# Kernel optimization log

Measured on AMD Instinct MI355X. Metric: run time of the kernel, lower is better.

## Reference

```python
import jax, jax.numpy as jnp
import numpy as np

B, S, D, H = 2, 2048, 1024, 16
DK = D // H


def setup_inputs() -> dict:
    key = jax.random.key(0)
    ks = jax.random.split(key, 12)
    sd = 1.0 / np.sqrt(D)
    inp = {
        "query": jax.random.normal(ks[0], (B, S, D), jnp.float32),
        "key": jax.random.normal(ks[1], (B, S, D), jnp.float32),
        "value": jax.random.normal(ks[2], (B, S, D), jnp.float32),
        # causal mask, broadcast over batch and heads: [1, 1, S, S]
        "mask": jnp.tril(jnp.ones((S, S), jnp.bool_))[None, None],
        "wq_w": jax.random.uniform(ks[3], (D, D), jnp.float32, -sd, sd),
        "wq_b": jax.random.uniform(ks[4], (D,), jnp.float32, -sd, sd),
        "wk_w": jax.random.uniform(ks[5], (D, D), jnp.float32, -sd, sd),
        "wk_b": jax.random.uniform(ks[6], (D,), jnp.float32, -sd, sd),
        "wv_w": jax.random.uniform(ks[7], (D, D), jnp.float32, -sd, sd),
        "wv_b": jax.random.uniform(ks[8], (D,), jnp.float32, -sd, sd),
        "wo_w": jax.random.uniform(ks[9], (D, D), jnp.float32, -sd, sd),
        "wo_b": jax.random.uniform(ks[10], (D,), jnp.float32, -sd, sd),
    }
    return inp


def reference(query, key, value, mask, wq_w, wq_b, wk_w, wk_b, wv_w, wv_b, wo_w, wo_b):
    # linear projections (torch Linear: x @ W^T + b), split into heads -> [B, H, S, DK]
    def proj(x, w, b):
        y = jnp.einsum("bsd,ed->bse", x, w) + b
        return y.reshape(B, S, H, DK).transpose(0, 2, 1, 3)

    q = proj(query, wq_w, wq_b)
    k = proj(key, wk_w, wk_b)
    v = proj(value, wv_w, wv_b)

    scale = 1.0 / np.sqrt(DK)
    scores = jnp.einsum("bhqd,bhkd->bhqk", q, k) * scale  # [B, H, S, S]
    scores = jnp.where(mask, scores, -jnp.inf)
    attn = jax.nn.softmax(scores, axis=-1)
    out = jnp.einsum("bhqk,bhkd->bhqd", attn, v)  # [B, H, S, DK]
    out = out.transpose(0, 2, 1, 3).reshape(B, S, D)
    # output projection; dropout is identity at eval / p=0
    return jnp.einsum("bsd,ed->bse", out, wo_w) + wo_b
```

## Files before the change

### kernel.cpp

```cpp
#include <hip/hip_runtime.h>


typedef unsigned short u16;
typedef __bf16 bf16x8 __attribute__((ext_vector_type(8)));
typedef float f32x4 __attribute__((ext_vector_type(4)));
typedef float f32x4v __attribute__((ext_vector_type(4)));
typedef u16 u16x4 __attribute__((ext_vector_type(4)));
typedef int i32x4 __attribute__((ext_vector_type(4)));

#define B_ 2
#define S_ 2048
#define D_ 1024
#define H_ 16
#define DK_ 64

__device__ __forceinline__ u16 f2bf(float f) {
  __bf16 h = (__bf16)f;
  return __builtin_bit_cast(u16, h);
}

__device__ __forceinline__ float fexp2(float x) {
  return __builtin_amdgcn_exp2f(x);
}

__device__ __forceinline__ f32x4 mfma16(bf16x8 a, bf16x8 b, f32x4 c) {
  return __builtin_amdgcn_mfma_f32_16x16x32_bf16(a, b, c, 0, 0, 0);
}

typedef __attribute__((address_space(1))) void GV;
typedef __attribute__((address_space(3))) void LV;
__device__ __forceinline__ void gload16(const u16* g, u16* l) {
  __builtin_amdgcn_global_load_lds((GV*)g, (LV*)l, 16, 0, 0);
}

__global__ __launch_bounds__(256) void cast_all(const float* __restrict__ s0, const float* __restrict__ s1,
                                                const float* __restrict__ s2, const float* __restrict__ s3,
                                                const float* __restrict__ s4, const float* __restrict__ s5,
                                                const float* __restrict__ s6, u16* __restrict__ dst) {
  const int N0 = 1048576, N1 = 2097152, N2 = 3145728, N3 = 3407872, N4 = 3670016, N5 = 3932160, N6 = 4194304;
  int stride = gridDim.x * blockDim.x;
  for (int i = blockIdx.x * blockDim.x + threadIdx.x; i < N6; i += stride) {
    const float* src;
    int off;
    if (i < N0)      { src = s0; off = i; }
    else if (i < N1) { src = s1; off = i - N0; }
    else if (i < N2) { src = s2; off = i - N1; }
    else if (i < N3) { src = s3; off = i - N2; }
    else if (i < N4) { src = s4; off = i - N3; }
    else if (i < N5) { src = s5; off = i - N4; }
    else             { src = s6; off = i - N5; }
    f32x4v v = reinterpret_cast<const f32x4v*>(src)[off];
    u16x4 o;
    o.x = f2bf(v.x); o.y = f2bf(v.y); o.z = f2bf(v.z); o.w = f2bf(v.w);
    reinterpret_cast<u16x4*>(dst)[i] = o;
  }
}

__device__ __forceinline__ void gemm_tile_128(const u16* __restrict__ A,
                                              const u16* __restrict__ Bw,
                                              int K, int bm, int bn,
                                              f32x4 (&acc)[4][4],
                                              u16* ldsA, u16* ldsB) {
  const int tid = threadIdx.x;
  const int lane = tid & 63;
  const int w = tid >> 6;
  const int wm = w >> 1, wn = w & 1;
  const int fr = lane & 15, fq = lane >> 4;

  const u16* aBase = A + (size_t)(bm * 128) * K;
  const u16* bBase = Bw + (size_t)(bn * 128) * K;

  const int r0 = tid >> 2;
  const int cq0 = tid & 3;
  const int cs0 = (cq0 ^ (r0 & 3)) * 8;
  const int cs1 = (cq0 ^ ((r0 + 64) & 3)) * 8;

#define STAGE_G(buf, kk)                                                          \
  do {                                                                            \
    gload16(aBase + (size_t)r0 * K + (kk) + cs0, ldsA + (buf)*4096 + tid * 8);     \
    gload16(aBase + (size_t)(r0 + 64) * K + (kk) + cs1, ldsA + (buf)*4096 + (tid + 256) * 8); \
    gload16(bBase + (size_t)r0 * K + (kk) + cs0, ldsB + (buf)*4096 + tid * 8);     \
    gload16(bBase + (size_t)(r0 + 64) * K + (kk) + cs1, ldsB + (buf)*4096 + (tid + 256) * 8); \
  } while (0)

  STAGE_G(0, 0);
  __syncthreads();

  const int nk = K >> 5;
  for (int t = 0; t < nk; ++t) {
    const int cur = t & 1;
    if (t + 1 < nk) STAGE_G(cur ^ 1, (t + 1) * 32);
    const u16* la = ldsA + cur * 4096;
    const u16* lb = ldsB + cur * 4096;
    bf16x8 af[4], bfv[4];
#pragma unroll
    for (int m = 0; m < 4; ++m) {
      int row = wm * 64 + m * 16 + fr;
      int cq = fq ^ (row & 3);
      af[m] = *reinterpret_cast<const bf16x8*>(la + (row * 4 + cq) * 8);
    }
#pragma unroll
    for (int n = 0; n < 4; ++n) {
      int row = wn * 64 + n * 16 + fr;
      int cq = fq ^ (row & 3);
      bfv[n] = *reinterpret_cast<const bf16x8*>(lb + (row * 4 + cq) * 8);
    }
    __builtin_amdgcn_s_setprio(1);
#pragma unroll
    for (int m = 0; m < 4; ++m)
#pragma unroll
      for (int n = 0; n < 4; ++n)
        acc[m][n] = mfma16(af[m], bfv[n], acc[m][n]);
    __builtin_amdgcn_s_setprio(0);
    __syncthreads();
  }
#undef STAGE_G
}

__global__ __launch_bounds__(256) void gemm_qkv(const u16* __restrict__ Xq, const u16* __restrict__ Xk,
                                                const u16* __restrict__ Xv, const u16* __restrict__ Wq,
                                                const u16* __restrict__ Wk, const u16* __restrict__ Wv,
                                                const float* __restrict__ bq, const float* __restrict__ bk,
                                                const float* __restrict__ bv,
                                                u16* __restrict__ Qw, u16* __restrict__ Kw,
                                                u16* __restrict__ Vt) {
  __shared__ __align__(16) u16 ldsA[2 * 128 * 32];
  __shared__ __align__(16) u16 ldsB[2 * 128 * 32];
  const int z = blockIdx.z;
  const u16* A = (z == 0) ? Xq : (z == 1) ? Xk : Xv;
  const u16* W = (z == 0) ? Wq : (z == 1) ? Wk : Wv;
  const float* bias = (z == 0) ? bq : (z == 1) ? bk : bv;
  const float osc = (z == 0) ? (0.125f * 1.44269504f) : 1.0f;

  f32x4 acc[4][4];
#pragma unroll
  for (int m = 0; m < 4; ++m)
#pragma unroll
    for (int n = 0; n < 4; ++n)
      acc[m][n] = (f32x4){0.f, 0.f, 0.f, 0.f};

  gemm_tile_128(A, W, 1024, blockIdx.y, blockIdx.x, acc, ldsA, ldsB);

  const int lane = threadIdx.x & 63;
  const int w = threadIdx.x >> 6, wm = w >> 1, wn = w & 1;
  const int fr = lane & 15, fq = lane >> 4;
#pragma unroll
  for (int m = 0; m < 4; ++m) {
#pragma unroll
    for (int n = 0; n < 4; ++n) {
      int col = blockIdx.x * 128 + wn * 64 + n * 16 + fr;
      float bcol = bias[col];
      int h = col >> 6, dk = col & 63;
#pragma unroll
      for (int j = 0; j < 4; ++j) {
        int row = blockIdx.y * 128 + wm * 64 + m * 16 + fq * 4 + j;
        float v = (acc[m][n][j] + bcol) * osc;
        u16 bb = f2bf(v);
        int b = row >> 11, s = row & (S_ - 1);
        if (z == 0)      Qw[((b * H_ + h) * S_ + s) * DK_ + dk] = bb;
        else if (z == 1) Kw[((b * H_ + h) * S_ + s) * DK_ + dk] = bb;
        else             Vt[((b * H_ + h) * DK_ + dk) * S_ + s] = bb;
      }
    }
  }
}

__global__ __launch_bounds__(256) void gemm_out(const u16* __restrict__ O, const u16* __restrict__ Wo,
                                                const float* __restrict__ bo, float* __restrict__ Y) {
  __shared__ __align__(16) u16 ldsA[2 * 128 * 32];
  __shared__ __align__(16) u16 ldsB[2 * 128 * 32];
  f32x4 acc[4][4];
#pragma unroll
  for (int m = 0; m < 4; ++m)
#pragma unroll
    for (int n = 0; n < 4; ++n)
      acc[m][n] = (f32x4){0.f, 0.f, 0.f, 0.f};

  gemm_tile_128(O, Wo, 1024, blockIdx.y, blockIdx.x, acc, ldsA, ldsB);

  const int lane = threadIdx.x & 63;
  const int w = threadIdx.x >> 6, wm = w >> 1, wn = w & 1;
  const int fr = lane & 15, fq = lane >> 4;
#pragma unroll
  for (int m = 0; m < 4; ++m) {
#pragma unroll
    for (int n = 0; n < 4; ++n) {
      int col = blockIdx.x * 128 + wn * 64 + n * 16 + fr;
      float bcol = bo[col];
#pragma unroll
      for (int j = 0; j < 4; ++j) {
        int row = blockIdx.y * 128 + wm * 64 + m * 16 + fq * 4 + j;
        Y[(size_t)row * D_ + col] = acc[m][n][j] + bcol;
      }
    }
  }
}

__global__ __launch_bounds__(256) void attn_kernel(const u16* __restrict__ Qw,
                                                   const u16* __restrict__ Kw,
                                                   const u16* __restrict__ Vt,
                                                   u16* __restrict__ O) {
  __shared__ __align__(16) u16 Kl[2][64 * 64];
  __shared__ __align__(16) u16 Vl[2][64 * 64];
  __shared__ __align__(16) u16 Pl[4 * 16 * 72];

  const int id = blockIdx.x;
  const int bh = (id & 7) | (((id >> 3) & 3) << 3);
  const int pair = id >> 5;

  const int tid = threadIdx.x, lane = tid & 63, w = tid >> 6;
  const int fr = lane & 15, fq = lane >> 4;

  const u16* Kg = Kw + (size_t)bh * S_ * DK_;
  const u16* Vg = Vt + (size_t)bh * DK_ * S_;
  const int b = bh >> 4, h = bh & 15;

  const int sr = tid >> 3;
  const int sc = (tid & 7) * 8;
  const int l0 = (sr * 64 + sc) ^ ((sr & 7) << 3);
  const int l1 = ((sr + 32) * 64 + sc) ^ ((sr & 7) << 3);

  const bf16x8 ones = {(__bf16)1.f, (__bf16)1.f, (__bf16)1.f, (__bf16)1.f,
                       (__bf16)1.f, (__bf16)1.f, (__bf16)1.f, (__bf16)1.f};

#pragma unroll
  for (int half = 0; half < 2; ++half) {
    const int qb = half ? (31 - pair) : pair;
    const int nkv = qb + 1;
    const u16* Qg = Qw + ((size_t)bh * S_ + qb * 64) * DK_;

    bf16x8 qa[2];
#pragma unroll
    for (int kh = 0; kh < 2; ++kh)
      qa[kh] = *reinterpret_cast<const bf16x8*>(Qg + (w * 16 + fr) * DK_ + kh * 32 + fq * 8);

    f32x4 o[4], ol;
#pragma unroll
    for (int n = 0; n < 4; ++n) o[n] = (f32x4){0.f, 0.f, 0.f, 0.f};
    ol = (f32x4){0.f, 0.f, 0.f, 0.f};

    i32x4 rk0 = *reinterpret_cast<const i32x4*>(Kg + (size_t)sr * DK_ + sc);
    i32x4 rk1 = *reinterpret_cast<const i32x4*>(Kg + (size_t)(sr + 32) * DK_ + sc);
    i32x4 rv0 = *reinterpret_cast<const i32x4*>(Vg + (size_t)sr * S_ + sc);
    i32x4 rv1 = *reinterpret_cast<const i32x4*>(Vg + (size_t)(sr + 32) * S_ + sc);

    for (int kv = 0; kv < nkv; ++kv) {
      const int cur = kv & 1;
      *reinterpret_cast<i32x4*>(&Kl[cur][l0]) = rk0;
      *reinterpret_cast<i32x4*>(&Kl[cur][l1]) = rk1;
      *reinterpret_cast<i32x4*>(&Vl[cur][l0]) = rv0;
      *reinterpret_cast<i32x4*>(&Vl[cur][l1]) = rv1;
      if (kv + 1 < nkv) {
        const u16* kn = Kg + (size_t)((kv + 1) * 64 + sr) * DK_ + sc;
        const u16* vn = Vg + (size_t)sr * S_ + (kv + 1) * 64 + sc;
        rk0 = *reinterpret_cast<const i32x4*>(kn);
        rk1 = *reinterpret_cast<const i32x4*>(kn + 32 * DK_);
        rv0 = *reinterpret_cast<const i32x4*>(vn);
        rv1 = *reinterpret_cast<const i32x4*>(vn + 32 * S_);
      }
      __syncthreads();

      f32x4 s[4];
#pragma unroll
      for (int n = 0; n < 4; ++n) s[n] = (f32x4){0.f, 0.f, 0.f, 0.f};
      __builtin_amdgcn_s_setprio(1);
#pragma unroll
      for (int n = 0; n < 4; ++n) {
#pragma unroll
        for (int kh = 0; kh < 2; ++kh) {
          int row = n * 16 + fr;
          int e = (row * 64 + kh * 32 + fq * 8) ^ ((row & 7) << 3);
          bf16x8 kb = *reinterpret_cast<const bf16x8*>(&Kl[cur][e]);
          s[n] = mfma16(qa[kh], kb, s[n]);
        }
      }
      __builtin_amdgcn_s_setprio(0);

      if (kv == qb) {
        const int qrow_base = qb * 64 + w * 16 + fq * 4;
#pragma unroll
        for (int n = 0; n < 4; ++n) {
          int col = kv * 64 + n * 16 + fr;
#pragma unroll
          for (int j = 0; j < 4; ++j)
            if (col > qrow_base + j) s[n][j] = -1.0e30f;
        }
      }
#pragma unroll
      for (int n = 0; n < 4; ++n)
#pragma unroll
        for (int j = 0; j < 4; ++j)
          s[n][j] = fexp2(s[n][j]);

      u16* pw = &Pl[w * 16 * 72];
#pragma unroll
      for (int j = 0; j < 4; ++j)
#pragma unroll
        for (int n = 0; n < 4; ++n)
          pw[(fq * 4 + j) * 72 + n * 16 + fr] = f2bf(s[n][j]);
      asm volatile("s_waitcnt lgkmcnt(0)" ::: "memory");

      bf16x8 pa[2];
#pragma unroll
      for (int kh = 0; kh < 2; ++kh)
        pa[kh] = *reinterpret_cast<const bf16x8*>(&pw[fr * 72 + kh * 32 + fq * 8]);

      __builtin_amdgcn_s_setprio(1);
#pragma unroll
      for (int n = 0; n < 4; ++n) {
#pragma unroll
        for (int kh = 0; kh < 2; ++kh) {
          int row = n * 16 + fr;
          int e = (row * 64 + kh * 32 + fq * 8) ^ ((row & 7) << 3);
          bf16x8 vb = *reinterpret_cast<const bf16x8*>(&Vl[cur][e]);
          o[n] = mfma16(pa[kh], vb, o[n]);
        }
      }
      ol = mfma16(pa[0], ones, ol);
      ol = mfma16(pa[1], ones, ol);
      __builtin_amdgcn_s_setprio(0);
    }

#pragma unroll
    for (int j = 0; j < 4; ++j) {
      float inv = 1.f / ol[j];
      int s_idx = qb * 64 + w * 16 + fq * 4 + j;
      size_t base = ((size_t)b * S_ + s_idx) * D_ + h * 64;
#pragma unroll
      for (int n = 0; n < 4; ++n)
        O[base + n * 16 + fr] = f2bf(o[n][j] * inv);
    }
    __syncthreads();
  }
}

extern "C" void kernel_launch(void* const* d_in, const int* in_sizes, int n_in,
                              void* d_out, int out_size, void* d_ws, size_t ws_size,
                              hipStream_t stream) {
  const float* q_in = (const float*)d_in[0];
  const float* k_in = (const float*)d_in[1];
  const float* v_in = (const float*)d_in[2];
  const float* wq = (const float*)d_in[4];
  const float* bq = (const float*)d_in[5];
  const float* wk = (const float*)d_in[6];
  const float* bk = (const float*)d_in[7];
  const float* wv = (const float*)d_in[8];
  const float* bv = (const float*)d_in[9];
  const float* wo = (const float*)d_in[10];
  const float* bo = (const float*)d_in[11];

  char* ws = (char*)d_ws;
  const size_t MB = 1024 * 1024;
  u16* Xq = (u16*)(ws + 0 * MB);
  u16* Xk = (u16*)(ws + 8 * MB);
  u16* Xv = (u16*)(ws + 16 * MB);
  u16* Wq = (u16*)(ws + 24 * MB);
  u16* Wk = (u16*)(ws + 26 * MB);
  u16* Wv = (u16*)(ws + 28 * MB);
  u16* Wo = (u16*)(ws + 30 * MB);
  u16* Qw = (u16*)(ws + 32 * MB);
  u16* Kw = (u16*)(ws + 40 * MB);
  u16* Vt = (u16*)(ws + 48 * MB);
  u16* Ob = (u16*)(ws + 0 * MB);

  cast_all<<<2048, 256, 0, stream>>>(q_in, k_in, v_in, wq, wk, wv, wo, (u16*)ws);
  gemm_qkv<<<dim3(8, 32, 3), 256, 0, stream>>>(Xq, Xk, Xv, Wq, Wk, Wv, bq, bk, bv, Qw, Kw, Vt);
  attn_kernel<<<512, 256, 0, stream>>>(Qw, Kw, Vt, Ob);
  gemm_out<<<dim3(8, 32), 256, 0, stream>>>(Ob, Wo, bo, (float*)d_out);
}
```

Measured before the change: 127.3 us.

## Split attention KV across waves with 32x32 MFMA and triple-buffer GEMM loads

The attention kernel is rewritten so each block handles one 64-row query tile. The four waves split the KV tiles between them and each reads K/V straight from global memory, using 32x32x16 MFMAs with in-register P repacking through cvt_pk and lane shuffles. The partial outputs and row sums are then combined through an LDS reduction tree, with twice as many blocks launched. Separately, the shared GEMM tile moves from double to triple buffering with vmcnt-based waits and one barrier per iteration. The goal is better load balance and less LDS and synchronisation traffic, at the cost of more global K/V reads and extra reduction work.

```diff
diff --git a/kernel.cpp b/kernel.cpp
--- a/kernel.cpp
+++ b/kernel.cpp
@@ -2,10 +2,14 @@
 
 
 typedef unsigned short u16;
+typedef unsigned int u32;
 typedef __bf16 bf16x8 __attribute__((ext_vector_type(8)));
 typedef float f32x4 __attribute__((ext_vector_type(4)));
+typedef float f32x16 __attribute__((ext_vector_type(16)));
+typedef float f32x2 __attribute__((ext_vector_type(2)));
 typedef float f32x4v __attribute__((ext_vector_type(4)));
 typedef u16 u16x4 __attribute__((ext_vector_type(4)));
+typedef u32 u32x4 __attribute__((ext_vector_type(4)));
 typedef int i32x4 __attribute__((ext_vector_type(4)));
 
 #define B_ 2
@@ -19,13 +23,21 @@
   return __builtin_bit_cast(u16, h);
 }
 
-__device__ __forceinline__ float fexp2(float x) {
-  return __builtin_amdgcn_exp2f(x);
-}
+__device__ __forceinline__ float fexp2(float x) { return __builtin_amdgcn_exp2f(x); }
 
 __device__ __forceinline__ f32x4 mfma16(bf16x8 a, bf16x8 b, f32x4 c) {
   return __builtin_amdgcn_mfma_f32_16x16x32_bf16(a, b, c, 0, 0, 0);
 }
+__device__ __forceinline__ f32x16 mfma32(bf16x8 a, bf16x8 b, f32x16 c) {
+  return __builtin_amdgcn_mfma_f32_32x32x16_bf16(a, b, c, 0, 0, 0);
+}
+
+__device__ __forceinline__ u32 cvtpk(float lo, float hi) {
+  u32 r;
+  asm volatile("v_cvt_pk_bf16_f32 %0, %1, %2" : "=v"(r) : "v"(lo), "v"(hi));
+  return r;
+}
+__device__ __forceinline__ u32 sx32(u32 v) { return (u32)__shfl_xor((int)v, 32, 64); }
 
 typedef __attribute__((address_space(1))) void GV;
 typedef __attribute__((address_space(3))) void LV;
@@ -75,23 +87,29 @@
   const int cs0 = (cq0 ^ (r0 & 3)) * 8;
   const int cs1 = (cq0 ^ ((r0 + 64) & 3)) * 8;
 
-#define STAGE_G(buf, kk)                                                          \
-  do {                                                                            \
-    gload16(aBase + (size_t)r0 * K + (kk) + cs0, ldsA + (buf)*4096 + tid * 8);     \
-    gload16(aBase + (size_t)(r0 + 64) * K + (kk) + cs1, ldsA + (buf)*4096 + (tid + 256) * 8); \
-    gload16(bBase + (size_t)r0 * K + (kk) + cs0, ldsB + (buf)*4096 + tid * 8);     \
-    gload16(bBase + (size_t)(r0 + 64) * K + (kk) + cs1, ldsB + (buf)*4096 + (tid + 256) * 8); \
+#define STAGE_G(buf, kk)                                                                          \
+  do {                                                                                            \
+    gload16(aBase + (size_t)r0 * K + (kk) + cs0, ldsA + (buf) * 4096 + tid * 8);                  \
+    gload16(aBase + (size_t)(r0 + 64) * K + (kk) + cs1, ldsA + (buf) * 4096 + (tid + 256) * 8);   \
+    gload16(bBase + (size_t)r0 * K + (kk) + cs0, ldsB + (buf) * 4096 + tid * 8);                  \
+    gload16(bBase + (size_t)(r0 + 64) * K + (kk) + cs1, ldsB + (buf) * 4096 + (tid + 256) * 8);   \
   } while (0)
 
   STAGE_G(0, 0);
-  __syncthreads();
+  STAGE_G(1, 32);
 
   const int nk = K >> 5;
   for (int t = 0; t < nk; ++t) {
-    const int cur = t & 1;
-    if (t + 1 < nk) STAGE_G(cur ^ 1, (t + 1) * 32);
-    const u16* la = ldsA + cur * 4096;
-    const u16* lb = ldsB + cur * 4096;
+    if (t + 1 < nk) { asm volatile("s_waitcnt vmcnt(4)" ::: "memory"); }
+    else            { asm volatile("s_waitcnt vmcnt(0)" ::: "memory"); }
+    __builtin_amdgcn_s_barrier();
+    __builtin_amdgcn_sched_barrier(0);
+    if (t + 2 < nk) {
+      const int nb = (t + 2) % 3;
+      STAGE_G(nb, (t + 2) * 32);
+    }
+    const u16* la = ldsA + (t % 3) * 4096;
+    const u16* lb = ldsB + (t % 3) * 4096;
     bf16x8 af[4], bfv[4];
 #pragma unroll
     for (int m = 0; m < 4; ++m) {
@@ -112,7 +130,6 @@
       for (int n = 0; n < 4; ++n)
         acc[m][n] = mfma16(af[m], bfv[n], acc[m][n]);
     __builtin_amdgcn_s_setprio(0);
-    __syncthreads();
   }
 #undef STAGE_G
 }
@@ -124,8 +141,8 @@
                                                 const float* __restrict__ bv,
                                                 u16* __restrict__ Qw, u16* __restrict__ Kw,
                                                 u16* __restrict__ Vt) {
-  __shared__ __align__(16) u16 ldsA[2 * 128 * 32];
-  __shared__ __align__(16) u16 ldsB[2 * 128 * 32];
+  __shared__ __align__(16) u16 ldsA[3 * 128 * 32];
+  __shared__ __align__(16) u16 ldsB[3 * 128 * 32];
   const int z = blockIdx.z;
   const u16* A = (z == 0) ? Xq : (z == 1) ? Xk : Xv;
   const u16* W = (z == 0) ? Wq : (z == 1) ? Wk : Wv;
@@ -167,8 +184,8 @@
 
 __global__ __launch_bounds__(256) void gemm_out(const u16* __restrict__ O, const u16* __restrict__ Wo,
                                                 const float* __restrict__ bo, float* __restrict__ Y) {
-  __shared__ __align__(16) u16 ldsA[2 * 128 * 32];
-  __shared__ __align__(16) u16 ldsB[2 * 128 * 32];
+  __shared__ __align__(16) u16 ldsA[3 * 128 * 32];
+  __shared__ __align__(16) u16 ldsB[3 * 128 * 32];
   f32x4 acc[4][4];
 #pragma unroll
   for (int m = 0; m < 4; ++m)
@@ -200,137 +217,154 @@
                                                    const u16* __restrict__ Kw,
                                                    const u16* __restrict__ Vt,
                                                    u16* __restrict__ O) {
-  __shared__ __align__(16) u16 Kl[2][64 * 64];
-  __shared__ __align__(16) u16 Vl[2][64 * 64];
-  __shared__ __align__(16) u16 Pl[4 * 16 * 72];
+  __shared__ float mbuf[2][64][64];
+  __shared__ float mlbuf[2][64];
 
   const int id = blockIdx.x;
-  const int bh = (id & 7) | (((id >> 3) & 3) << 3);
-  const int pair = id >> 5;
-
-  const int tid = threadIdx.x, lane = tid & 63, w = tid >> 6;
-  const int fr = lane & 15, fq = lane >> 4;
-
+  const int bh = (id & 7) * 4 + ((id >> 3) & 3);
+  const int qb = 31 - (id >> 5);
+  const int tid = threadIdx.x;
+  const int w = tid >> 6;
+  const int lane = tid & 63;
+  const int col = lane & 31;
+  const int hi = lane >> 5;
+
+  const u16* Qg = Qw + ((size_t)bh * S_ + qb * 64) * DK_;
   const u16* Kg = Kw + (size_t)bh * S_ * DK_;
   const u16* Vg = Vt + (size_t)bh * DK_ * S_;
   const int b = bh >> 4, h = bh & 15;
 
-  const int sr = tid >> 3;
-  const int sc = (tid & 7) * 8;
-  const int l0 = (sr * 64 + sc) ^ ((sr & 7) << 3);
-  const int l1 = ((sr + 32) * 64 + sc) ^ ((sr & 7) << 3);
-
-  const bf16x8 ones = {(__bf16)1.f, (__bf16)1.f, (__bf16)1.f, (__bf16)1.f,
-                       (__bf16)1.f, (__bf16)1.f, (__bf16)1.f, (__bf16)1.f};
-
-#pragma unroll
-  for (int half = 0; half < 2; ++half) {
-    const int qb = half ? (31 - pair) : pair;
-    const int nkv = qb + 1;
-    const u16* Qg = Qw + ((size_t)bh * S_ + qb * 64) * DK_;
-
-    bf16x8 qa[2];
-#pragma unroll
-    for (int kh = 0; kh < 2; ++kh)
-      qa[kh] = *reinterpret_cast<const bf16x8*>(Qg + (w * 16 + fr) * DK_ + kh * 32 + fq * 8);
-
-    f32x4 o[4], ol;
-#pragma unroll
-    for (int n = 0; n < 4; ++n) o[n] = (f32x4){0.f, 0.f, 0.f, 0.f};
-    ol = (f32x4){0.f, 0.f, 0.f, 0.f};
-
-    i32x4 rk0 = *reinterpret_cast<const i32x4*>(Kg + (size_t)sr * DK_ + sc);
-    i32x4 rk1 = *reinterpret_cast<const i32x4*>(Kg + (size_t)(sr + 32) * DK_ + sc);
-    i32x4 rv0 = *reinterpret_cast<const i32x4*>(Vg + (size_t)sr * S_ + sc);
-    i32x4 rv1 = *reinterpret_cast<const i32x4*>(Vg + (size_t)(sr + 32) * S_ + sc);
-
-    for (int kv = 0; kv < nkv; ++kv) {
-      const int cur = kv & 1;
-      *reinterpret_cast<i32x4*>(&Kl[cur][l0]) = rk0;
-      *reinterpret_cast<i32x4*>(&Kl[cur][l1]) = rk1;
-      *reinterpret_cast<i32x4*>(&Vl[cur][l0]) = rv0;
-      *reinterpret_cast<i32x4*>(&Vl[cur][l1]) = rv1;
-      if (kv + 1 < nkv) {
-        const u16* kn = Kg + (size_t)((kv + 1) * 64 + sr) * DK_ + sc;
-        const u16* vn = Vg + (size_t)sr * S_ + (kv + 1) * 64 + sc;
-        rk0 = *reinterpret_cast<const i32x4*>(kn);
-        rk1 = *reinterpret_cast<const i32x4*>(kn + 32 * DK_);
-        rv0 = *reinterpret_cast<const i32x4*>(vn);
-        rv1 = *reinterpret_cast<const i32x4*>(vn + 32 * S_);
-      }
-      __syncthreads();
-
-      f32x4 s[4];
-#pragma unroll
-      for (int n = 0; n < 4; ++n) s[n] = (f32x4){0.f, 0.f, 0.f, 0.f};
+  bf16x8 qf[2][4];
+#pragma unroll
+  for (int qt = 0; qt < 2; ++qt)
+#pragma unroll
+    for (int c = 0; c < 4; ++c)
+      qf[qt][c] = *reinterpret_cast<const bf16x8*>(Qg + (qt * 32 + col) * DK_ + c * 16 + hi * 8);
+
+  f32x16 o[2][2];
+  float ll[2] = {0.f, 0.f};
+#pragma unroll
+  for (int qt = 0; qt < 2; ++qt)
+#pragma unroll
+    for (int dt = 0; dt < 2; ++dt)
+#pragma unroll
+      for (int r = 0; r < 16; ++r) o[qt][dt][r] = 0.f;
+
+  for (int t = w; t <= qb; t += 4) {
+    const u16* Kt = Kg + (size_t)t * 64 * DK_;
+    const u16* Vtt = Vg + t * 64;
+    bf16x8 pa[2][4];
+#pragma unroll
+    for (int kt = 0; kt < 2; ++kt) {
+      bf16x8 ka[4];
+#pragma unroll
+      for (int c = 0; c < 4; ++c)
+        ka[c] = *reinterpret_cast<const bf16x8*>(Kt + (kt * 32 + col) * DK_ + c * 16 + hi * 8);
+      f32x16 s0, s1;
+#pragma unroll
+      for (int r = 0; r < 16; ++r) { s0[r] = 0.f; s1[r] = 0.f; }
       __builtin_amdgcn_s_setprio(1);
 #pragma unroll
-      for (int n = 0; n < 4; ++n) {
-#pragma unroll
-        for (int kh = 0; kh < 2; ++kh) {
-          int row = n * 16 + fr;
-          int e = (row * 64 + kh * 32 + fq * 8) ^ ((row & 7) << 3);
-          bf16x8 kb = *reinterpret_cast<const bf16x8*>(&Kl[cur][e]);
-          s[n] = mfma16(qa[kh], kb, s[n]);
+      for (int c = 0; c < 4; ++c) {
+        s0 = mfma32(ka[c], qf[0][c], s0);
+        s1 = mfma32(ka[c], qf[1][c], s1);
+      }
+      __builtin_amdgcn_s_setprio(0);
+
+      if (t == qb) {
+#pragma unroll
+        for (int r = 0; r < 16; ++r) {
+          int krow = kt * 32 + (r & 3) + 8 * (r >> 2) + 4 * hi;
+          if (krow > col) s0[r] = -1.0e30f;
+          if (krow > 32 + col) s1[r] = -1.0e30f;
         }
       }
-      __builtin_amdgcn_s_setprio(0);
-
-      if (kv == qb) {
-        const int qrow_base = qb * 64 + w * 16 + fq * 4;
-#pragma unroll
-        for (int n = 0; n < 4; ++n) {
-          int col = kv * 64 + n * 16 + fr;
-#pragma unroll
-          for (int j = 0; j < 4; ++j)
-            if (col > qrow_base + j) s[n][j] = -1.0e30f;
-        }
-      }
-#pragma unroll
-      for (int n = 0; n < 4; ++n)
-#pragma unroll
-        for (int j = 0; j < 4; ++j)
-          s[n][j] = fexp2(s[n][j]);
-
-      u16* pw = &Pl[w * 16 * 72];
-#pragma unroll
-      for (int j = 0; j < 4; ++j)
-#pragma unroll
-        for (int n = 0; n < 4; ++n)
-          pw[(fq * 4 + j) * 72 + n * 16 + fr] = f2bf(s[n][j]);
-      asm volatile("s_waitcnt lgkmcnt(0)" ::: "memory");
-
-      bf16x8 pa[2];
-#pragma unroll
-      for (int kh = 0; kh < 2; ++kh)
-        pa[kh] = *reinterpret_cast<const bf16x8*>(&pw[fr * 72 + kh * 32 + fq * 8]);
-
-      __builtin_amdgcn_s_setprio(1);
-#pragma unroll
-      for (int n = 0; n < 4; ++n) {
-#pragma unroll
-        for (int kh = 0; kh < 2; ++kh) {
-          int row = n * 16 + fr;
-          int e = (row * 64 + kh * 32 + fq * 8) ^ ((row & 7) << 3);
-          bf16x8 vb = *reinterpret_cast<const bf16x8*>(&Vl[cur][e]);
-          o[n] = mfma16(pa[kh], vb, o[n]);
-        }
-      }
-      ol = mfma16(pa[0], ones, ol);
-      ol = mfma16(pa[1], ones, ol);
-      __builtin_amdgcn_s_setprio(0);
-    }
-
-#pragma unroll
-    for (int j = 0; j < 4; ++j) {
-      float inv = 1.f / ol[j];
-      int s_idx = qb * 64 + w * 16 + fq * 4 + j;
-      size_t base = ((size_t)b * S_ + s_idx) * D_ + h * 64;
-#pragma unroll
-      for (int n = 0; n < 4; ++n)
-        O[base + n * 16 + fr] = f2bf(o[n][j] * inv);
-    }
-    __syncthreads();
+      float a0 = 0.f, a1 = 0.f;
+#pragma unroll
+      for (int r = 0; r < 16; ++r) {
+        s0[r] = fexp2(s0[r]); a0 += s0[r];
+        s1[r] = fexp2(s1[r]); a1 += s1[r];
+      }
+      ll[0] += a0; ll[1] += a1;
+
+#pragma unroll
+      for (int qt = 0; qt < 2; ++qt) {
+        const f32x16& sv = qt ? s1 : s0;
+        u32 g0 = cvtpk(sv[0], sv[1]),   g1 = cvtpk(sv[2], sv[3]);
+        u32 g2 = cvtpk(sv[4], sv[5]),   g3 = cvtpk(sv[6], sv[7]);
+        u32 g4 = cvtpk(sv[8], sv[9]),   g5 = cvtpk(sv[10], sv[11]);
+        u32 g6 = cvtpk(sv[12], sv[13]), g7 = cvtpk(sv[14], sv[15]);
+        u32 t0 = sx32(g0), t1 = sx32(g1), t2 = sx32(g2), t3 = sx32(g3);
+        u32 t4 = sx32(g4), t5 = sx32(g5), t6 = sx32(g6), t7 = sx32(g7);
+        u32x4 lo4, hi4;
+        lo4.x = hi ? t2 : g0;  lo4.y = hi ? t3 : g1;
+        lo4.z = hi ? g2 : t0;  lo4.w = hi ? g3 : t1;
+        hi4.x = hi ? t6 : g4;  hi4.y = hi ? t7 : g5;
+        hi4.z = hi ? g6 : t4;  hi4.w = hi ? g7 : t5;
+        pa[qt][kt * 2 + 0] = __builtin_bit_cast(bf16x8, lo4);
+        pa[qt][kt * 2 + 1] = __builtin_bit_cast(bf16x8, hi4);
+      }
+    }
+
+    __builtin_amdgcn_s_setprio(1);
+#pragma unroll
+    for (int dt = 0; dt < 2; ++dt) {
+#pragma unroll
+      for (int kc = 0; kc < 4; ++kc) {
+        bf16x8 vb = *reinterpret_cast<const bf16x8*>(Vtt + (size_t)(dt * 32 + col) * S_ + kc * 16 + hi * 8);
+        o[0][dt] = mfma32(pa[0][kc], vb, o[0][dt]);
+        o[1][dt] = mfma32(pa[1][kc], vb, o[1][dt]);
+      }
+    }
+    __builtin_amdgcn_s_setprio(0);
+  }
+
+  ll[0] += __shfl_xor(ll[0], 32, 64);
+  ll[1] += __shfl_xor(ll[1], 32, 64);
+
+#define WRITE_PART(i)                                                         \
+  do {                                                                        \
+    _Pragma("unroll") for (int qt = 0; qt < 2; ++qt) {                        \
+      _Pragma("unroll") for (int dt = 0; dt < 2; ++dt)                        \
+        _Pragma("unroll") for (int r = 0; r < 16; ++r) {                      \
+          int qrow = qt * 32 + (r & 3) + 8 * (r >> 2) + 4 * hi;               \
+          mbuf[i][qrow][dt * 32 + col] = o[qt][dt][r];                        \
+        }                                                                     \
+      if (hi == 0) mlbuf[i][qt * 32 + col] = ll[qt];                          \
+    }                                                                         \
+  } while (0)
+#define ADD_PART(i)                                                           \
+  do {                                                                        \
+    _Pragma("unroll") for (int qt = 0; qt < 2; ++qt) {                        \
+      _Pragma("unroll") for (int dt = 0; dt < 2; ++dt)                        \
+        _Pragma("unroll") for (int r = 0; r < 16; ++r) {                      \
+          int qrow = qt * 32 + (r & 3) + 8 * (r >> 2) + 4 * hi;               \
+          o[qt][dt][r] += mbuf[i][qrow][dt * 32 + col];                       \
+        }                                                                     \
+      ll[qt] += mlbuf[i][qt * 32 + col];                                      \
+    }                                                                         \
+  } while (0)
+
+  if (w == 1) WRITE_PART(0);
+  if (w == 3) WRITE_PART(1);
+  __syncthreads();
+  if (w == 0) ADD_PART(0);
+  if (w == 2) ADD_PART(1);
+  __syncthreads();
+  if (w == 2) WRITE_PART(0);
+  __syncthreads();
+  if (w == 0) { ADD_PART(0); WRITE_PART(0); }
+  __syncthreads();
+#undef WRITE_PART
+#undef ADD_PART
+
+#pragma unroll
+  for (int it = 0; it < 8; ++it) {
+    int q = w * 16 + it * 2 + hi;
+    f32x2 v = *reinterpret_cast<const f32x2*>(&mbuf[0][q][col * 2]);
+    float linv = 1.f / mlbuf[0][q];
+    u32 pk = cvtpk(v.x * linv, v.y * linv);
+    *reinterpret_cast<u32*>(O + ((size_t)b * S_ + qb * 64 + q) * D_ + h * 64 + col * 2) = pk;
   }
 }
 
@@ -365,6 +399,6 @@
 
   cast_all<<<2048, 256, 0, stream>>>(q_in, k_in, v_in, wq, wk, wv, wo, (u16*)ws);
   gemm_qkv<<<dim3(8, 32, 3), 256, 0, stream>>>(Xq, Xk, Xv, Wq, Wk, Wv, bq, bk, bv, Qw, Kw, Vt);
-  attn_kernel<<<512, 256, 0, stream>>>(Qw, Kw, Vt, Ob);
+  attn_kernel<<<1024, 256, 0, stream>>>(Qw, Kw, Vt, Ob);
   gemm_out<<<dim3(8, 32), 256, 0, stream>>>(Ob, Wo, bo, (float*)d_out);
 }
```

Result: slower. 132.8 us (+4.4%).
